# Kernel tuning notes

Hardware: AMD Instinct MI355X
Metric: run time of the kernel (lower is better)

Reference implementation:

```python
import jax, jax.numpy as jnp
import numpy as np

NUM_NODES = 10000
NUM_EDGES = 640000
IN_CH = 128
HID = 128
OUT_CH = 1


def setup_inputs() -> dict:
    key = jax.random.key(0)
    ks = jax.random.split(key, 12)
    x = jax.random.normal(ks[0], (NUM_NODES, IN_CH), dtype=jnp.float32)
    edge_index = jax.random.randint(ks[1], (2, NUM_EDGES), 0, NUM_NODES, dtype=jnp.int64)
    edge_weight = jax.random.uniform(ks[2], (NUM_EDGES,), dtype=jnp.float32)
    s1 = 1.0 / np.sqrt(IN_CH)
    s2 = 1.0 / np.sqrt(HID)
    W1 = jax.random.uniform(ks[3], (HID, IN_CH), minval=-s1, maxval=s1, dtype=jnp.float32)
    b1 = jnp.zeros((HID,), dtype=jnp.float32)
    W2 = jax.random.uniform(ks[4], (HID, HID), minval=-s2, maxval=s2, dtype=jnp.float32)
    b2 = jnp.zeros((HID,), dtype=jnp.float32)
    sc = 1.0 / np.sqrt(HID * 3)
    conv_w = jax.random.uniform(ks[5], (HID, HID, 3), minval=-sc, maxval=sc, dtype=jnp.float32)
    conv_b = jax.random.uniform(ks[6], (HID,), minval=-sc, maxval=sc, dtype=jnp.float32)
    fc_w = jax.random.uniform(ks[7], (OUT_CH, HID), minval=-s2, maxval=s2, dtype=jnp.float32)
    fc_b = jax.random.uniform(ks[8], (OUT_CH,), minval=-s2, maxval=s2, dtype=jnp.float32)
    return {"x": x, "edge_index": edge_index, "edge_weight": edge_weight,
            "W1": W1, "b1": b1, "W2": W2, "b2": b2,
            "conv_w": conv_w, "conv_b": conv_b, "fc_w": fc_w, "fc_b": fc_b}


def _gcn_conv(x, row, col, norm, W, b):
    # PyG GCNConv: linear (no bias in lin), normalized scatter-add, then bias
    xw = x @ W.T                                   # [N, out]
    msg = xw[row] * norm[:, None]                  # gather + edge scale [E, out]
    out = jax.ops.segment_sum(msg, col, num_segments=NUM_NODES)
    return out + b


def reference(x, edge_index, edge_weight, W1, b1, W2, b2, conv_w, conv_b, fc_w, fc_b):
    # gcn_norm with self-loops (fill_value=1.0)
    loop = jnp.arange(NUM_NODES, dtype=edge_index.dtype)
    row = jnp.concatenate([edge_index[0], loop])
    col = jnp.concatenate([edge_index[1], loop])
    w = jnp.concatenate([edge_weight, jnp.ones((NUM_NODES,), dtype=edge_weight.dtype)])
    deg = jax.ops.segment_sum(w, col, num_segments=NUM_NODES)
    dinv = jnp.where(deg > 0, jax.lax.rsqrt(deg), 0.0)
    norm = dinv[row] * w * dinv[col]

    h = jax.nn.relu(_gcn_conv(x, row, col, norm, W1, b1))
    # dropout is identity in eval mode
    h = jax.nn.relu(_gcn_conv(h, row, col, norm, W2, b2))

    # temporal conv1d over node axis: [N,H] -> [1,H,N]
    hc = h.T[None, :, :]
    hc = jax.lax.conv_general_dilated(hc, conv_w, window_strides=(1,),
                                      padding='SAME',
                                      dimension_numbers=('NCH', 'OIH', 'NCH'))
    hc = hc + conv_b[None, :, None]
    h = hc[0].T                                    # [N, H]

    return (h @ fc_w.T + fc_b).squeeze()           # [N]
```

## Files before the change

### kernel.cpp

```cpp
#include <hip/hip_runtime.h>
#include <hip/hip_bf16.h>

#define N_NODES 10000
#define N_EDGES 640000
#define CH 128
#define NB 128
#define EPB (N_EDGES / NB)
#define NCHUNK 40

__global__ __launch_bounds__(256) void hist_kernel(const int* __restrict__ ei,
                                                   const float* __restrict__ ew,
                                                   int* __restrict__ hist,
                                                   float* __restrict__ dhist) {
    __shared__ int h[N_NODES];
    __shared__ float hf[N_NODES];
    int b = blockIdx.x, t = threadIdx.x;
    for (int i = t; i < N_NODES; i += 256) { h[i] = 0; hf[i] = 0.0f; }
    __syncthreads();
    int e0 = b * EPB;
    for (int i = t; i < EPB; i += 256) {
        int c = ei[N_EDGES + e0 + i];
        float w = ew[e0 + i];
        atomicAdd(&h[c], 1);
        atomicAdd(&hf[c], w);
    }
    __syncthreads();
    for (int i = t; i < N_NODES; i += 256) {
        hist[b * N_NODES + i] = h[i];
        dhist[b * N_NODES + i] = hf[i];
    }
}

__global__ __launch_bounds__(256) void reduce_kernel(const int* __restrict__ hist,
        const float* __restrict__ dhist, int* __restrict__ tot,
        float* __restrict__ dinv, int* __restrict__ csum,
        const float* __restrict__ conv_w, const float* __restrict__ conv_b,
        const float* __restrict__ fc_w, const float* __restrict__ fc_b,
        float* __restrict__ vbuf, float* __restrict__ c0) {
    int blk = blockIdx.x, t = threadIdx.x;
    if (blk == NCHUNK) {
        for (int i = t; i <= 384; i += 256) {
            if (i < 384) {
                float s = 0.0f;
                for (int o = 0; o < CH; ++o) s += fc_w[o] * conv_w[o * 384 + i];
                vbuf[i] = s;
            } else {
                float s = fc_b[0];
                for (int o = 0; o < CH; ++o) s += fc_w[o] * conv_b[o];
                *c0 = s;
            }
        }
        return;
    }
    int n = blk * 256 + t;
    int c = 0;
    if (n < N_NODES) {
        float d = 0.0f;
        #pragma unroll 4
        for (int b = 0; b < NB; ++b) {
            c += hist[b * N_NODES + n];
            d += dhist[b * N_NODES + n];
        }
        tot[n] = c;
        dinv[n] = rsqrtf(d + 1.0f);
    }
    __shared__ int wred[4];
    int lane = t & 63, wave = t >> 6;
    int s = c;
    #pragma unroll
    for (int off = 32; off > 0; off >>= 1) s += __shfl_down(s, off, 64);
    if (lane == 0) wred[wave] = s;
    __syncthreads();
    if (t == 0) csum[blk] = wred[0] + wred[1] + wred[2] + wred[3];
}

__global__ __launch_bounds__(256) void bofs_kernel(int* __restrict__ hist,
        const int* __restrict__ tot, const int* __restrict__ csum,
        int* __restrict__ offs) {
    __shared__ int lds_csum[NCHUNK];
    __shared__ int wsum[4];
    int blk = blockIdx.x, t = threadIdx.x;
    if (t < NCHUNK) lds_csum[t] = csum[t];
    __syncthreads();
    int base = 0;
    for (int i = 0; i < blk; ++i) base += lds_csum[i];
    int n = blk * 256 + t;
    int v = (n < N_NODES) ? tot[n] : 0;
    int lane = t & 63, wave = t >> 6;
    int s = v;
    #pragma unroll
    for (int off = 1; off < 64; off <<= 1) {
        int u = __shfl_up(s, off, 64);
        if (lane >= off) s += u;
    }
    if (lane == 63) wsum[wave] = s;
    __syncthreads();
    int wbase = 0;
    for (int i = 0; i < wave; ++i) wbase += wsum[i];
    if (n < N_NODES) {
        int run = base + wbase + s - v;
        offs[n] = run;
        for (int b = 0; b < NB; ++b) {
            int h = hist[b * N_NODES + n];
            hist[b * N_NODES + n] = run;
            run += h;
        }
    }
}

__global__ __launch_bounds__(256) void scatter_kernel(const int* __restrict__ ei,
        const float* __restrict__ ew, const float* __restrict__ dinv,
        const int* __restrict__ bofs, int2* __restrict__ erec) {
    __shared__ int cur[N_NODES];
    __shared__ float di[N_NODES];
    int b = blockIdx.x, t = threadIdx.x;
    for (int i = t; i < N_NODES; i += 256) {
        cur[i] = bofs[b * N_NODES + i];
        di[i] = dinv[i];
    }
    __syncthreads();
    int e0 = b * EPB;
    for (int i = t; i < EPB; i += 256) {
        int e = e0 + i;
        int r = ei[e];
        int c = ei[N_EDGES + e];
        int p = atomicAdd(&cur[c], 1);
        float v = di[r] * ew[e] * di[c];
        erec[p] = make_int2(r, __float_as_int(v));
    }
}

__global__ __launch_bounds__(256) void gemm128_kernel(const float* __restrict__ A,
                                                      const float* __restrict__ W,
                                                      float* __restrict__ out, int M) {
    __shared__ float As[32][68];
    __shared__ float Ws[32][132];
    int tid = threadIdx.x;
    int tx = tid & 31;
    int ty = tid >> 5;
    int row0 = blockIdx.x * 64;
    float acc[8][4] = {};
    for (int k0 = 0; k0 < 128; k0 += 32) {
        #pragma unroll
        for (int i = 0; i < 8; ++i) {
            int idx = tid + i * 256;
            int r = idx >> 5, k = idx & 31;
            int gr = row0 + r;
            As[k][r] = (gr < M) ? A[gr * CH + k0 + k] : 0.0f;
        }
        #pragma unroll
        for (int i = 0; i < 16; ++i) {
            int idx = tid + i * 256;
            int o = idx >> 5, k = idx & 31;
            Ws[k][o] = W[o * CH + k0 + k];
        }
        __syncthreads();
        #pragma unroll
        for (int kk = 0; kk < 32; ++kk) {
            float a[8], w[4];
            #pragma unroll
            for (int j = 0; j < 8; ++j) a[j] = As[kk][ty * 8 + j];
            #pragma unroll
            for (int c = 0; c < 4; ++c) w[c] = Ws[kk][tx * 4 + c];
            #pragma unroll
            for (int j = 0; j < 8; ++j)
                #pragma unroll
                for (int c = 0; c < 4; ++c)
                    acc[j][c] += a[j] * w[c];
        }
        __syncthreads();
    }
    #pragma unroll
    for (int j = 0; j < 8; ++j) {
        int gr = row0 + ty * 8 + j;
        if (gr < M) {
            float4 v = make_float4(acc[j][0], acc[j][1], acc[j][2], acc[j][3]);
            *reinterpret_cast<float4*>(&out[gr * CH + tx * 4]) = v;
        }
    }
}

__global__ __launch_bounds__(256) void agg_kernel(const float4* __restrict__ xw4,
        const int2* __restrict__ erec, const int* __restrict__ offs,
        const int* __restrict__ cnt, const float* __restrict__ dinv,
        const float4* __restrict__ bias4, float4* __restrict__ out4) {
    int l = threadIdx.x & 31;
    int g = threadIdx.x >> 5;
    int n = blockIdx.x * 8 + g;
    float d = dinv[n];
    float dd = d * d;
    float4 self = xw4[n * 32 + l];
    float4 acc = make_float4(dd * self.x, dd * self.y, dd * self.z, dd * self.w);
    int start = offs[n];
    int num = cnt[n];
    int i = 0;
    for (; i + 8 <= num; i += 8) {
        int2 r[8];
        #pragma unroll
        for (int j = 0; j < 8; ++j) r[j] = erec[start + i + j];
        float4 f[8];
        #pragma unroll
        for (int j = 0; j < 8; ++j) f[j] = xw4[r[j].x * 32 + l];
        #pragma unroll
        for (int j = 0; j < 8; ++j) {
            float v = __int_as_float(r[j].y);
            acc.x += v * f[j].x; acc.y += v * f[j].y;
            acc.z += v * f[j].z; acc.w += v * f[j].w;
        }
    }
    for (; i < num; ++i) {
        int2 r = erec[start + i];
        float4 f = xw4[r.x * 32 + l];
        float v = __int_as_float(r.y);
        acc.x += v * f.x; acc.y += v * f.y; acc.z += v * f.z; acc.w += v * f.w;
    }
    float4 bb = bias4[l];
    acc.x = fmaxf(acc.x + bb.x, 0.0f);
    acc.y = fmaxf(acc.y + bb.y, 0.0f);
    acc.z = fmaxf(acc.z + bb.z, 0.0f);
    acc.w = fmaxf(acc.w + bb.w, 0.0f);
    out4[n * 32 + l] = acc;
}

__global__ __launch_bounds__(128) void convfc_kernel(const float* __restrict__ h,
        const float* __restrict__ v, const float* __restrict__ c0,
        float* __restrict__ out, int N) {
    int n = blockIdx.x;
    int t = threadIdx.x;
    float p = 0.0f;
    if (n > 0)     p += h[(n - 1) * CH + t] * v[t * 3 + 0];
    p += h[n * CH + t] * v[t * 3 + 1];
    if (n < N - 1) p += h[(n + 1) * CH + t] * v[t * 3 + 2];
    #pragma unroll
    for (int off = 32; off > 0; off >>= 1) p += __shfl_down(p, off, 64);
    __shared__ float red[2];
    if ((t & 63) == 0) red[t >> 6] = p;
    __syncthreads();
    if (t == 0) out[n] = red[0] + red[1] + *c0;
}

extern "C" void kernel_launch(void* const* d_in, const int* in_sizes, int n_in,
                              void* d_out, int out_size, void* d_ws, size_t ws_size,
                              hipStream_t stream) {
    const float* x       = (const float*)d_in[0];
    const int*   ei      = (const int*)d_in[1];
    const float* ew      = (const float*)d_in[2];
    const float* W1      = (const float*)d_in[3];
    const float* b1      = (const float*)d_in[4];
    const float* W2      = (const float*)d_in[5];
    const float* b2      = (const float*)d_in[6];
    const float* conv_w  = (const float*)d_in[7];
    const float* conv_b  = (const float*)d_in[8];
    const float* fc_w    = (const float*)d_in[9];
    const float* fc_b    = (const float*)d_in[10];
    float* out = (float*)d_out;

    float* bufA   = (float*)d_ws;
    float* bufB   = bufA + N_NODES * CH;
    int2*  erec   = (int2*)(bufB + N_NODES * CH);
    int*   hist   = (int*)bufA;
    float* dhist  = (float*)erec;
    int*   tot    = (int*)(erec + N_EDGES);
    int*   offs   = tot + N_NODES;
    float* dinv   = (float*)(offs + N_NODES);
    float* vbuf   = dinv + N_NODES;
    float* c0     = vbuf + 384;
    int*   csum   = (int*)(c0 + 1);

    hist_kernel<<<NB, 256, 0, stream>>>(ei, ew, hist, dhist);
    reduce_kernel<<<NCHUNK + 1, 256, 0, stream>>>(hist, dhist, tot, dinv, csum,
                                                  conv_w, conv_b, fc_w, fc_b, vbuf, c0);
    bofs_kernel<<<NCHUNK, 256, 0, stream>>>(hist, tot, csum, offs);
    scatter_kernel<<<NB, 256, 0, stream>>>(ei, ew, dinv, hist, erec);

    const int gemm_grid = (N_NODES + 63) / 64;
    gemm128_kernel<<<gemm_grid, 256, 0, stream>>>(x, W1, bufA, N_NODES);
    agg_kernel<<<N_NODES / 8, 256, 0, stream>>>((const float4*)bufA, erec, offs, tot,
                                                dinv, (const float4*)b1, (float4*)bufB);
    gemm128_kernel<<<gemm_grid, 256, 0, stream>>>(bufB, W2, bufA, N_NODES);
    agg_kernel<<<N_NODES / 8, 256, 0, stream>>>((const float4*)bufA, erec, offs, tot,
                                                dinv, (const float4*)b2, (float4*)bufB);
    convfc_kernel<<<N_NODES, 128, 0, stream>>>(bufB, vbuf, c0, out, N_NODES);
}
```

Measured before the change: 229.2 us.

## Fuse histogram with first GEMM, compute degree from CSR, restructure normalization

The count histogram is merged with the first GEMM into one launch, so the independent GEMM blocks can overlap the atomic histogram work. The weighted-degree histogram is dropped; degrees are instead summed per node from the CSR edge records in a new deg_kernel. The per-edge normalization moves into the aggregation, which now gathers dinv[row] per edge and scales by dinv[col] at the end. Other changes: NB doubles, the hist buffer is relocated, and convfc processes four nodes per block without shared memory. The cost is an extra launch and an extra gathered load per edge in each aggregation.

```diff
diff --git a/kernel.cpp b/kernel.cpp
--- a/kernel.cpp
+++ b/kernel.cpp
@@ -4,36 +4,76 @@
 #define N_NODES 10000
 #define N_EDGES 640000
 #define CH 128
-#define NB 128
+#define NB 256
 #define EPB (N_EDGES / NB)
 #define NCHUNK 40
 
-__global__ __launch_bounds__(256) void hist_kernel(const int* __restrict__ ei,
-                                                   const float* __restrict__ ew,
-                                                   int* __restrict__ hist,
-                                                   float* __restrict__ dhist) {
-    __shared__ int h[N_NODES];
-    __shared__ float hf[N_NODES];
-    int b = blockIdx.x, t = threadIdx.x;
-    for (int i = t; i < N_NODES; i += 256) { h[i] = 0; hf[i] = 0.0f; }
-    __syncthreads();
-    int e0 = b * EPB;
-    for (int i = t; i < EPB; i += 256) {
-        int c = ei[N_EDGES + e0 + i];
-        float w = ew[e0 + i];
-        atomicAdd(&h[c], 1);
-        atomicAdd(&hf[c], w);
-    }
-    __syncthreads();
-    for (int i = t; i < N_NODES; i += 256) {
-        hist[b * N_NODES + i] = h[i];
-        dhist[b * N_NODES + i] = hf[i];
+__global__ __launch_bounds__(256) void fused_hist_gemm(const int* __restrict__ ei,
+        const float* __restrict__ x, const float* __restrict__ W1,
+        int* __restrict__ hist, float* __restrict__ out) {
+    __shared__ __align__(16) char smem[40000];
+    int t = threadIdx.x;
+    if (blockIdx.x < NB) {
+        int* h = (int*)smem;
+        int b = blockIdx.x;
+        for (int i = t; i < N_NODES; i += 256) h[i] = 0;
+        __syncthreads();
+        int e0 = b * EPB;
+        for (int i = t; i < EPB; i += 256)
+            atomicAdd(&h[ei[N_EDGES + e0 + i]], 1);
+        __syncthreads();
+        for (int i = t; i < N_NODES; i += 256)
+            hist[b * N_NODES + i] = h[i];
+        return;
+    }
+    float (*As)[68]  = (float(*)[68])smem;
+    float (*Ws)[132] = (float(*)[132])(smem + 32 * 68 * sizeof(float));
+    int tx = t & 31;
+    int ty = t >> 5;
+    int row0 = (blockIdx.x - NB) * 64;
+    float acc[8][4] = {};
+    for (int k0 = 0; k0 < 128; k0 += 32) {
+        #pragma unroll
+        for (int i = 0; i < 8; ++i) {
+            int idx = t + i * 256;
+            int r = idx >> 5, k = idx & 31;
+            int gr = row0 + r;
+            As[k][r] = (gr < N_NODES) ? x[gr * CH + k0 + k] : 0.0f;
+        }
+        #pragma unroll
+        for (int i = 0; i < 16; ++i) {
+            int idx = t + i * 256;
+            int o = idx >> 5, k = idx & 31;
+            Ws[k][o] = W1[o * CH + k0 + k];
+        }
+        __syncthreads();
+        #pragma unroll
+        for (int kk = 0; kk < 32; ++kk) {
+            float a[8], w[4];
+            #pragma unroll
+            for (int j = 0; j < 8; ++j) a[j] = As[kk][ty * 8 + j];
+            #pragma unroll
+            for (int c = 0; c < 4; ++c) w[c] = Ws[kk][tx * 4 + c];
+            #pragma unroll
+            for (int j = 0; j < 8; ++j)
+                #pragma unroll
+                for (int c = 0; c < 4; ++c)
+                    acc[j][c] += a[j] * w[c];
+        }
+        __syncthreads();
+    }
+    #pragma unroll
+    for (int j = 0; j < 8; ++j) {
+        int gr = row0 + ty * 8 + j;
+        if (gr < N_NODES) {
+            float4 v = make_float4(acc[j][0], acc[j][1], acc[j][2], acc[j][3]);
+            *reinterpret_cast<float4*>(&out[gr * CH + tx * 4]) = v;
+        }
     }
 }
 
 __global__ __launch_bounds__(256) void reduce_kernel(const int* __restrict__ hist,
-        const float* __restrict__ dhist, int* __restrict__ tot,
-        float* __restrict__ dinv, int* __restrict__ csum,
+        int* __restrict__ tot, int* __restrict__ csum,
         const float* __restrict__ conv_w, const float* __restrict__ conv_b,
         const float* __restrict__ fc_w, const float* __restrict__ fc_b,
         float* __restrict__ vbuf, float* __restrict__ c0) {
@@ -55,14 +95,9 @@
     int n = blk * 256 + t;
     int c = 0;
     if (n < N_NODES) {
-        float d = 0.0f;
-        #pragma unroll 4
-        for (int b = 0; b < NB; ++b) {
-            c += hist[b * N_NODES + n];
-            d += dhist[b * N_NODES + n];
-        }
+        #pragma unroll 8
+        for (int b = 0; b < NB; ++b) c += hist[b * N_NODES + n];
         tot[n] = c;
-        dinv[n] = rsqrtf(d + 1.0f);
     }
     __shared__ int wred[4];
     int lane = t & 63, wave = t >> 6;
@@ -109,15 +144,11 @@
 }
 
 __global__ __launch_bounds__(256) void scatter_kernel(const int* __restrict__ ei,
-        const float* __restrict__ ew, const float* __restrict__ dinv,
-        const int* __restrict__ bofs, int2* __restrict__ erec) {
+        const float* __restrict__ ew, const int* __restrict__ bofs,
+        int2* __restrict__ erec) {
     __shared__ int cur[N_NODES];
-    __shared__ float di[N_NODES];
     int b = blockIdx.x, t = threadIdx.x;
-    for (int i = t; i < N_NODES; i += 256) {
-        cur[i] = bofs[b * N_NODES + i];
-        di[i] = dinv[i];
-    }
+    for (int i = t; i < N_NODES; i += 256) cur[i] = bofs[b * N_NODES + i];
     __syncthreads();
     int e0 = b * EPB;
     for (int i = t; i < EPB; i += 256) {
@@ -125,9 +156,22 @@
         int r = ei[e];
         int c = ei[N_EDGES + e];
         int p = atomicAdd(&cur[c], 1);
-        float v = di[r] * ew[e] * di[c];
-        erec[p] = make_int2(r, __float_as_int(v));
-    }
+        erec[p] = make_int2(r, __float_as_int(ew[e]));
+    }
+}
+
+__global__ __launch_bounds__(256) void deg_kernel(const int2* __restrict__ erec,
+        const int* __restrict__ offs, const int* __restrict__ cnt,
+        float* __restrict__ dinv) {
+    int n = blockIdx.x * 8 + (threadIdx.x >> 5);
+    int l = threadIdx.x & 31;
+    int start = offs[n];
+    int num = cnt[n];
+    float s = 0.0f;
+    for (int i = l; i < num; i += 32) s += __int_as_float(erec[start + i].y);
+    #pragma unroll
+    for (int off = 16; off > 0; off >>= 1) s += __shfl_down(s, off, 32);
+    if (l == 0) dinv[n] = rsqrtf(s + 1.0f);
 }
 
 __global__ __launch_bounds__(256) void gemm128_kernel(const float* __restrict__ A,
@@ -188,9 +232,8 @@
     int g = threadIdx.x >> 5;
     int n = blockIdx.x * 8 + g;
     float d = dinv[n];
-    float dd = d * d;
     float4 self = xw4[n * 32 + l];
-    float4 acc = make_float4(dd * self.x, dd * self.y, dd * self.z, dd * self.w);
+    float4 acc = make_float4(d * self.x, d * self.y, d * self.z, d * self.w);
     int start = offs[n];
     int num = cnt[n];
     int i = 0;
@@ -199,11 +242,14 @@
         #pragma unroll
         for (int j = 0; j < 8; ++j) r[j] = erec[start + i + j];
         float4 f[8];
+        float dr[8];
         #pragma unroll
         for (int j = 0; j < 8; ++j) f[j] = xw4[r[j].x * 32 + l];
         #pragma unroll
+        for (int j = 0; j < 8; ++j) dr[j] = dinv[r[j].x];
+        #pragma unroll
         for (int j = 0; j < 8; ++j) {
-            float v = __int_as_float(r[j].y);
+            float v = __int_as_float(r[j].y) * dr[j];
             acc.x += v * f[j].x; acc.y += v * f[j].y;
             acc.z += v * f[j].z; acc.w += v * f[j].w;
         }
@@ -211,32 +257,32 @@
     for (; i < num; ++i) {
         int2 r = erec[start + i];
         float4 f = xw4[r.x * 32 + l];
-        float v = __int_as_float(r.y);
+        float v = __int_as_float(r.y) * dinv[r.x];
         acc.x += v * f.x; acc.y += v * f.y; acc.z += v * f.z; acc.w += v * f.w;
     }
     float4 bb = bias4[l];
-    acc.x = fmaxf(acc.x + bb.x, 0.0f);
-    acc.y = fmaxf(acc.y + bb.y, 0.0f);
-    acc.z = fmaxf(acc.z + bb.z, 0.0f);
-    acc.w = fmaxf(acc.w + bb.w, 0.0f);
+    acc.x = fmaxf(d * acc.x + bb.x, 0.0f);
+    acc.y = fmaxf(d * acc.y + bb.y, 0.0f);
+    acc.z = fmaxf(d * acc.z + bb.z, 0.0f);
+    acc.w = fmaxf(d * acc.w + bb.w, 0.0f);
     out4[n * 32 + l] = acc;
 }
 
-__global__ __launch_bounds__(128) void convfc_kernel(const float* __restrict__ h,
+__global__ __launch_bounds__(256) void convfc_kernel(const float* __restrict__ h,
         const float* __restrict__ v, const float* __restrict__ c0,
         float* __restrict__ out, int N) {
-    int n = blockIdx.x;
-    int t = threadIdx.x;
-    float p = 0.0f;
-    if (n > 0)     p += h[(n - 1) * CH + t] * v[t * 3 + 0];
-    p += h[n * CH + t] * v[t * 3 + 1];
-    if (n < N - 1) p += h[(n + 1) * CH + t] * v[t * 3 + 2];
+    int n = blockIdx.x * 4 + (threadIdx.x >> 6);
+    int l = threadIdx.x & 63;
+    if (n >= N) return;
+    const float* hn = h + n * CH;
+    float v0a = v[l * 3 + 0],        v1a = v[l * 3 + 1],        v2a = v[l * 3 + 2];
+    float v0b = v[(l + 64) * 3 + 0], v1b = v[(l + 64) * 3 + 1], v2b = v[(l + 64) * 3 + 2];
+    float p = hn[l] * v1a + hn[l + 64] * v1b;
+    if (n > 0)     p += hn[l - CH] * v0a + hn[l + 64 - CH] * v0b;
+    if (n < N - 1) p += hn[l + CH] * v2a + hn[l + 64 + CH] * v2b;
     #pragma unroll
     for (int off = 32; off > 0; off >>= 1) p += __shfl_down(p, off, 64);
-    __shared__ float red[2];
-    if ((t & 63) == 0) red[t >> 6] = p;
-    __syncthreads();
-    if (t == 0) out[n] = red[0] + red[1] + *c0;
+    if (l == 0) out[n] = p + *c0;
 }
 
 extern "C" void kernel_launch(void* const* d_in, const int* in_sizes, int n_in,
@@ -258,27 +304,27 @@
     float* bufA   = (float*)d_ws;
     float* bufB   = bufA + N_NODES * CH;
     int2*  erec   = (int2*)(bufB + N_NODES * CH);
-    int*   hist   = (int*)bufA;
-    float* dhist  = (float*)erec;
-    int*   tot    = (int*)(erec + N_EDGES);
+    int*   hist   = (int*)(erec + N_EDGES);
+    int*   tot    = hist + NB * N_NODES;
     int*   offs   = tot + N_NODES;
     float* dinv   = (float*)(offs + N_NODES);
     float* vbuf   = dinv + N_NODES;
     float* c0     = vbuf + 384;
     int*   csum   = (int*)(c0 + 1);
 
-    hist_kernel<<<NB, 256, 0, stream>>>(ei, ew, hist, dhist);
-    reduce_kernel<<<NCHUNK + 1, 256, 0, stream>>>(hist, dhist, tot, dinv, csum,
+    const int gemm_grid = (N_NODES + 63) / 64;
+
+    fused_hist_gemm<<<NB + gemm_grid, 256, 0, stream>>>(ei, x, W1, hist, bufA);
+    reduce_kernel<<<NCHUNK + 1, 256, 0, stream>>>(hist, tot, csum,
                                                   conv_w, conv_b, fc_w, fc_b, vbuf, c0);
     bofs_kernel<<<NCHUNK, 256, 0, stream>>>(hist, tot, csum, offs);
-    scatter_kernel<<<NB, 256, 0, stream>>>(ei, ew, dinv, hist, erec);
-
-    const int gemm_grid = (N_NODES + 63) / 64;
-    gemm128_kernel<<<gemm_grid, 256, 0, stream>>>(x, W1, bufA, N_NODES);
+    scatter_kernel<<<NB, 256, 0, stream>>>(ei, ew, hist, erec);
+    deg_kernel<<<N_NODES / 8, 256, 0, stream>>>(erec, offs, tot, dinv);
+
     agg_kernel<<<N_NODES / 8, 256, 0, stream>>>((const float4*)bufA, erec, offs, tot,
                                                 dinv, (const float4*)b1, (float4*)bufB);
     gemm128_kernel<<<gemm_grid, 256, 0, stream>>>(bufB, W2, bufA, N_NODES);
     agg_kernel<<<N_NODES / 8, 256, 0, stream>>>((const float4*)bufA, erec, offs, tot,
                                                 dinv, (const float4*)b2, (float4*)bufB);
-    convfc_kernel<<<N_NODES, 128, 0, stream>>>(bufB, vbuf, c0, out, N_NODES);
-}
+    convfc_kernel<<<(N_NODES + 3) / 4, 256, 0, stream>>>(bufB, vbuf, c0, out, N_NODES);
+}
```

After: 225.5 us. About the same (-1.6%).
